# Optimization experiments

Measured on AMD Instinct MI355X. Metric: run time of the kernel, lower is better.

The kernel has to match this reference:

```python
import jax, jax.numpy as jnp
import numpy as np

K = 2          # top-k experts per token
CVLOSS = 0.0
SWITCHLOSS = 0.01
ZLOSS = 0.001
EPS = 1e-6


def setup_inputs() -> dict:
    key = jax.random.key(0)
    ks = jax.random.split(key, 4)
    B, L, D, H, E = 4, 2048, 512, 1024, 8
    x = jax.random.normal(ks[0], (B, L, D), dtype=jnp.float32)
    w_gate = jax.random.normal(ks[1], (E, D), dtype=jnp.float32) * 0.02
    w1 = jax.random.normal(ks[2], (E, D, H), dtype=jnp.float32) * (1.0 / np.sqrt(D))
    b1 = jnp.zeros((E, H), dtype=jnp.float32)
    w2 = jax.random.normal(ks[3], (E, H, D), dtype=jnp.float32) * (1.0 / np.sqrt(H))
    b2 = jnp.zeros((E, D), dtype=jnp.float32)
    return {"x": x, "w_gate": w_gate, "w1": w1, "b1": b1, "w2": w2, "b2": b2}


def _moe_forward(x, w_gate, w1, b1, w2, b2):
    B, L, D = x.shape
    E = w_gate.shape[0]
    xf = x.reshape(-1, D)                      # [N, D]
    N = xf.shape[0]

    # --- top-k gating (eval path: sample_topk=0, no skip_mask, concat=False) ---
    logits = xf @ w_gate.T                     # [N, E]
    probs = jax.nn.softmax(logits, axis=1)
    top_k_gates, top_k_idx = jax.lax.top_k(probs, K)        # [N, K]
    denom = jax.lax.stop_gradient(top_k_gates.sum(axis=1, keepdims=True) + EPS)
    top_k_gates = top_k_gates / denom
    gates = jnp.zeros_like(probs).at[jnp.arange(N)[:, None], top_k_idx].set(top_k_gates)  # [N, E]

    # --- auxiliary losses ---
    psum = probs.sum(axis=0)
    psum_n = psum / psum.sum()                 # F.normalize(p=1)
    freqs = (gates > 0).astype(probs.dtype).sum(axis=0)
    freqs_n = freqs / freqs.sum()
    cv = jnp.var(psum_n, ddof=1) / (jnp.mean(psum_n) ** 2 + 1e-10)
    switch = (psum_n * freqs_n).sum() * E
    zl = jnp.mean(jax.nn.logsumexp(logits, axis=1) ** 2)
    loss = CVLOSS * cv + SWITCHLOSS * switch + ZLOSS * zl

    # --- dispatch / per-expert FFN / gate-weighted combine ---
    # Mathematically identical to SparseDispatcher: tokens with gates[n,e]==0
    # contribute exactly zero for expert e. Loop is over the small fixed set
    # of experts, keeping intermediates at [N, H] (as the original does per group).
    y = jnp.zeros_like(xf)
    for e in range(E):
        h = jax.nn.relu(xf @ w1[e] + b1[e])    # [N, H]
        y = y + gates[:, e:e + 1] * (h @ w2[e] + b2[e])
    return y.reshape(B, L, D), loss


def reference(x, w_gate, w1, b1, w2, b2):
    return _moe_forward(x, w_gate, w1, b1, w2, b2)
```

## Files before the change

kernel.cpp:

```cpp
#include <hip/hip_runtime.h>
#include <hip/hip_bf16.h>
#include <math.h>

#define NTOK 8192
#define DDIM 512
#define HDIM 1024
#define NEXP 8
#define TOPK 2
#define NBLK_GATE (NTOK / 4)

typedef __bf16 bf16;
typedef __attribute__((ext_vector_type(8))) __bf16 bf16x8;
typedef __attribute__((ext_vector_type(4))) float f32x4;

#define WS_PSUM_PART_OFF  4096
#define WS_ZL_PART_OFF    (WS_PSUM_PART_OFF + NBLK_GATE * NEXP * 4)
#define WS_GATES_OFF      (WS_ZL_PART_OFF + NBLK_GATE * 4)
#define WS_LIST_OFF       (WS_GATES_OFF + NTOK * TOPK * 4)
#define WS_XB_OFF         (WS_LIST_OFF + NEXP * NTOK * 4)
#define WS_W1T_OFF        (WS_XB_OFF + NTOK * DDIM * 2)
#define WS_W2T_OFF        (WS_W1T_OFF + NEXP * DDIM * HDIM * 2)
#define WS_HB_OFF         (WS_W2T_OFF + NEXP * DDIM * HDIM * 2)

#define GL2LDS(g, l) __builtin_amdgcn_global_load_lds( \
    (const __attribute__((address_space(1))) void*)(g), \
    (__attribute__((address_space(3))) void*)(l), 16, 0, 0)

__global__ __launch_bounds__(256)
void gate_kernel(const float* __restrict__ x, const float* __restrict__ wg,
                 int* __restrict__ counts, float* __restrict__ psum_part,
                 float* __restrict__ zl_part, float* __restrict__ gates,
                 int* __restrict__ list, bf16* __restrict__ xb) {
    __shared__ float wls[NEXP * DDIM];
    __shared__ float blk_psum[NEXP];
    __shared__ float blk_zl;
    const int t = threadIdx.x;

    for (int i = t; i < NEXP * DDIM / 4; i += 256)
        ((float4*)wls)[i] = ((const float4*)wg)[i];
    if (t < NEXP) blk_psum[t] = 0.f;
    if (t == 0) blk_zl = 0.f;
    __syncthreads();

    const int wave = t >> 6, lane = t & 63;
    const int n = blockIdx.x * 4 + wave;

    const float* xr = x + (size_t)n * DDIM;

    {
        const float4 v0 = ((const float4*)xr)[lane * 2];
        const float4 v1 = ((const float4*)xr)[lane * 2 + 1];
        bf16x8 bv;
        bv[0] = (bf16)v0.x; bv[1] = (bf16)v0.y; bv[2] = (bf16)v0.z; bv[3] = (bf16)v0.w;
        bv[4] = (bf16)v1.x; bv[5] = (bf16)v1.y; bv[6] = (bf16)v1.z; bv[7] = (bf16)v1.w;
        *(bf16x8*)(xb + (size_t)n * DDIM + lane * 8) = bv;
    }

    float acc[NEXP];
#pragma unroll
    for (int e = 0; e < NEXP; ++e) acc[e] = 0.f;
#pragma unroll
    for (int it = 0; it < DDIM / 64; ++it) {
        const float xv = xr[lane + 64 * it];
#pragma unroll
        for (int e = 0; e < NEXP; ++e)
            acc[e] = fmaf(xv, wls[e * DDIM + lane + 64 * it], acc[e]);
    }
#pragma unroll
    for (int e = 0; e < NEXP; ++e) {
#pragma unroll
        for (int off = 32; off > 0; off >>= 1)
            acc[e] += __shfl_xor(acc[e], off);
    }

    float m = acc[0];
#pragma unroll
    for (int e = 1; e < NEXP; ++e) m = fmaxf(m, acc[e]);
    float p[NEXP];
    float se = 0.f;
#pragma unroll
    for (int e = 0; e < NEXP; ++e) { p[e] = expf(acc[e] - m); se += p[e]; }
    const float lse = m + logf(se);
    const float inv = 1.f / se;
#pragma unroll
    for (int e = 0; e < NEXP; ++e) p[e] *= inv;

    int e0 = 0; float g0 = p[0];
#pragma unroll
    for (int e = 1; e < NEXP; ++e) if (p[e] > g0) { g0 = p[e]; e0 = e; }
    int e1 = -1; float g1 = -1.f;
#pragma unroll
    for (int e = 0; e < NEXP; ++e) if (e != e0 && p[e] > g1) { g1 = p[e]; e1 = e; }
    const float denom = g0 + g1 + 1e-6f;

    if (lane == 0) {
        gates[n * 2 + 0] = g0 / denom;
        gates[n * 2 + 1] = g1 / denom;
        const int p0 = atomicAdd(&counts[e0 * 64], 1);
        list[e0 * NTOK + p0] = n * 2 + 0;
        const int p1 = atomicAdd(&counts[e1 * 64], 1);
        list[e1 * NTOK + p1] = n * 2 + 1;
#pragma unroll
        for (int e = 0; e < NEXP; ++e) atomicAdd(&blk_psum[e], p[e]);
        atomicAdd(&blk_zl, lse * lse);
    }
    __syncthreads();
    if (t < NEXP) psum_part[blockIdx.x * NEXP + t] = blk_psum[t];
    if (t == 0) zl_part[blockIdx.x] = blk_zl;
}

template <int R, int C>
__global__ __launch_bounds__(256)
void transpose_cvt(const float* __restrict__ in, bf16* __restrict__ outp) {
    __shared__ float tile[32][33];
    const int e = blockIdx.z;
    const int x0 = blockIdx.x * 32;
    const int y0 = blockIdx.y * 32;
    const int tx = threadIdx.x & 31, ty = threadIdx.x >> 5;
    const float* ip = in + (size_t)e * R * C;
    bf16* op = outp + (size_t)e * R * C;
#pragma unroll
    for (int q = 0; q < 4; ++q)
        tile[ty + q * 8][tx] = ip[(size_t)(y0 + ty + q * 8) * C + x0 + tx];
    __syncthreads();
#pragma unroll
    for (int q = 0; q < 4; ++q)
        op[(size_t)(x0 + ty + q * 8) * R + y0 + tx] = (bf16)tile[tx][ty + q * 8];
}

template <int KD, int ND, bool PASS2>
__global__ __launch_bounds__(256)
void ffn_mfma(const bf16* __restrict__ A_src, const bf16* __restrict__ Wt,
              const float* __restrict__ bias, const int* __restrict__ counts,
              const int* __restrict__ list, const float* __restrict__ gates,
              float* __restrict__ y_out, bf16* __restrict__ h_out) {
    const int e = blockIdx.z;
    const int cnt = counts[e * 64];
    const int row0 = blockIdx.y * 128;
    if (row0 >= cnt) return;
    const int col0 = blockIdx.x * 128;

    __shared__ __align__(16) short As[2][128 * 64];
    __shared__ __align__(16) short Bs[2][128 * 64];
    __shared__ int   ls_entry[128];
    __shared__ float ls_gate[128];

    const int t = threadIdx.x;
    const int lane = t & 63;
    const int w = t >> 6;

    if (t < 128) {
        const int r = row0 + t;
        const int entry = (r < cnt) ? list[e * NTOK + r] : -1;
        ls_entry[t] = entry;
        ls_gate[t] = (PASS2 && entry >= 0) ? gates[entry] : 0.f;
    }
    __syncthreads();

    const int subrow = lane >> 3;
    const int swzoff = ((lane & 7) ^ subrow) * 16;
    const char* Ab = (const char*)A_src;
    const char* Bb = (const char*)Wt;
    size_t a_row_byte[4], b_row_byte[4];
#pragma unroll
    for (int q = 0; q < 4; ++q) {
        const int r = q * 32 + w * 8 + subrow;
        const int entry = ls_entry[r];
        const int src = entry < 0 ? 0 : (PASS2 ? entry : (entry >> 1));
        a_row_byte[q] = (size_t)src * KD * 2;
        b_row_byte[q] = ((size_t)e * ND + col0 + r) * KD * 2;
    }
    const int lds_wbase = w * 8 * 128;

    f32x4 acc[4][4];
#pragma unroll
    for (int i = 0; i < 4; ++i)
#pragma unroll
        for (int j = 0; j < 4; ++j) acc[i][j] = (f32x4){0.f, 0.f, 0.f, 0.f};

    const int rowblk = (w >> 1) * 64;
    const int colblk = (w & 1) * 64;
    const int fr = lane & 15;
    const int kg = lane >> 4;

    auto STAGE = [&](int buf, int k0) {
        const size_t koff = (size_t)k0 * 2 + swzoff;
        char* ab = (char*)As + buf * 16384 + lds_wbase;
        char* bb = (char*)Bs + buf * 16384 + lds_wbase;
#pragma unroll
        for (int q = 0; q < 4; ++q) {
            GL2LDS(Ab + a_row_byte[q] + koff, ab + q * 32 * 128);
            GL2LDS(Bb + b_row_byte[q] + koff, bb + q * 32 * 128);
        }
    };

    auto COMPUTE = [&](int buf) {
        const char* AsB = (const char*)As + buf * 16384;
        const char* BsB = (const char*)Bs + buf * 16384;
#pragma unroll
        for (int kk = 0; kk < 2; ++kk) {
            bf16x8 af[4], bg[4];
#pragma unroll
            for (int i = 0; i < 4; ++i) {
                const int ra = rowblk + i * 16 + fr;
                const int ca = (kk * 4 + kg) ^ (ra & 7);
                af[i] = *(const bf16x8*)(AsB + ra * 128 + ca * 16);
                const int rb = colblk + i * 16 + fr;
                const int cb = (kk * 4 + kg) ^ (rb & 7);
                bg[i] = *(const bf16x8*)(BsB + rb * 128 + cb * 16);
            }
#pragma unroll
            for (int i = 0; i < 4; ++i)
#pragma unroll
                for (int j = 0; j < 4; ++j)
                    acc[i][j] = __builtin_amdgcn_mfma_f32_16x16x32_bf16(
                        af[i], bg[j], acc[i][j], 0, 0, 0);
        }
    };

    constexpr int NT = KD / 64;
    STAGE(0, 0);
    __syncthreads();
    for (int kt = 0; kt < NT - 1; ++kt) {
        STAGE((kt + 1) & 1, (kt + 1) * 64);
        COMPUTE(kt & 1);
        __syncthreads();
    }
    COMPUTE((NT - 1) & 1);

    float bcol[4];
#pragma unroll
    for (int j = 0; j < 4; ++j)
        bcol[j] = bias[e * ND + col0 + colblk + j * 16 + fr];

#pragma unroll
    for (int i = 0; i < 4; ++i) {
#pragma unroll
        for (int rg = 0; rg < 4; ++rg) {
            const int r = rowblk + i * 16 + kg * 4 + rg;
            const int entry = ls_entry[r];
            if (entry < 0) continue;
            if (!PASS2) {
                bf16* hr = h_out + (size_t)entry * HDIM + col0 + colblk + fr;
#pragma unroll
                for (int j = 0; j < 4; ++j)
                    hr[j * 16] = (bf16)fmaxf(acc[i][j][rg] + bcol[j], 0.f);
            } else {
                const float g = ls_gate[r];
                float* yr = y_out + (size_t)(entry >> 1) * DDIM + col0 + colblk + fr;
#pragma unroll
                for (int j = 0; j < 4; ++j)
                    atomicAdd(&yr[j * 16], g * (acc[i][j][rg] + bcol[j]));
            }
        }
    }
}

__global__ __launch_bounds__(256)
void finalize_kernel(const int* __restrict__ counts,
                     const float* __restrict__ psum_part,
                     const float* __restrict__ zl_part,
                     float* __restrict__ outp) {
    __shared__ float sp[NEXP];
    __shared__ float sz;
    const int t = threadIdx.x;
    if (t < NEXP) sp[t] = 0.f;
    if (t == 0) sz = 0.f;
    __syncthreads();
    float pe[NEXP] = {0.f, 0.f, 0.f, 0.f, 0.f, 0.f, 0.f, 0.f};
    float z = 0.f;
    for (int b = t; b < NBLK_GATE; b += 256) {
#pragma unroll
        for (int e = 0; e < NEXP; ++e) pe[e] += psum_part[b * NEXP + e];
        z += zl_part[b];
    }
#pragma unroll
    for (int e = 0; e < NEXP; ++e) atomicAdd(&sp[e], pe[e]);
    atomicAdd(&sz, z);
    __syncthreads();
    if (t == 0) {
        float S = 0.f;
        for (int e = 0; e < NEXP; ++e) S += sp[e];
        const float F = (float)(NTOK * TOPK);
        float sw = 0.f;
        for (int e = 0; e < NEXP; ++e)
            sw += (sp[e] / S) * ((float)counts[e * 64] / F);
        sw *= (float)NEXP;
        const float zl = sz / (float)NTOK;
        outp[(size_t)NTOK * DDIM] = 0.01f * sw + 0.001f * zl;
    }
}

extern "C" void kernel_launch(void* const* d_in, const int* in_sizes, int n_in,
                              void* d_out, int out_size, void* d_ws, size_t ws_size,
                              hipStream_t stream) {
    (void)in_sizes; (void)n_in; (void)out_size; (void)ws_size;
    const float* x  = (const float*)d_in[0];
    const float* wg = (const float*)d_in[1];
    const float* w1 = (const float*)d_in[2];
    const float* b1 = (const float*)d_in[3];
    const float* w2 = (const float*)d_in[4];
    const float* b2 = (const float*)d_in[5];
    float* y = (float*)d_out;

    char* ws = (char*)d_ws;
    int*   counts    = (int*)(ws + 0);
    float* psum_part = (float*)(ws + WS_PSUM_PART_OFF);
    float* zl_part   = (float*)(ws + WS_ZL_PART_OFF);
    float* gates     = (float*)(ws + WS_GATES_OFF);
    int*   list      = (int*)(ws + WS_LIST_OFF);
    bf16*  xb        = (bf16*)(ws + WS_XB_OFF);
    bf16*  w1t       = (bf16*)(ws + WS_W1T_OFF);
    bf16*  w2t       = (bf16*)(ws + WS_W2T_OFF);
    bf16*  hb        = (bf16*)(ws + WS_HB_OFF);

    hipMemsetAsync(ws, 0, 4096, stream);
    hipMemsetAsync(d_out, 0, (size_t)NTOK * DDIM * sizeof(float), stream);

    transpose_cvt<DDIM, HDIM><<<dim3(HDIM / 32, DDIM / 32, NEXP), 256, 0, stream>>>(w1, w1t);
    transpose_cvt<HDIM, DDIM><<<dim3(DDIM / 32, HDIM / 32, NEXP), 256, 0, stream>>>(w2, w2t);

    gate_kernel<<<NBLK_GATE, 256, 0, stream>>>(x, wg, counts, psum_part, zl_part,
                                               gates, list, xb);

    ffn_mfma<DDIM, HDIM, false>
        <<<dim3(HDIM / 128, NTOK / 128, NEXP), 256, 0, stream>>>(
            xb, w1t, b1, counts, list, gates, nullptr, hb);

    ffn_mfma<HDIM, DDIM, true>
        <<<dim3(DDIM / 128, NTOK / 128, NEXP), 256, 0, stream>>>(
            hb, w2t, b2, counts, list, gates, y, nullptr);

    finalize_kernel<<<1, 256, 0, stream>>>(counts, psum_part, zl_part, y);
}
```

Baseline: 260.4 us.

## Pack routed tokens contiguously per expert and compact the FFN grid

Adds a plan kernel that builds per-expert cumulative offsets and a compact list of (expert, row-block) tiles, and a pack kernel that gathers routed token rows into a contiguous bf16 buffer in expert-sorted slot order. Both FFN GEMMs then launch only the needed row blocks (RBMAX) rather than a full NTOK/128 x NEXP grid of mostly empty blocks, and read contiguous A rows without per-row indirection. The list is stored as 16-bit indices. This adds two small launches, including a single-thread serial plan kernel, and per-row list and gate loads in the PASS2 epilogue.

```diff
diff --git a/kernel.cpp b/kernel.cpp
--- a/kernel.cpp
+++ b/kernel.cpp
@@ -7,20 +7,25 @@
 #define HDIM 1024
 #define NEXP 8
 #define TOPK 2
+#define TOTSLOT (NTOK * TOPK)
 #define NBLK_GATE (NTOK / 4)
+#define RBMAX 144
 
 typedef __bf16 bf16;
 typedef __attribute__((ext_vector_type(8))) __bf16 bf16x8;
 typedef __attribute__((ext_vector_type(4))) float f32x4;
 
+#define WS_CUMOFF_OFF     2048
+#define WS_RBE_OFF        2112
+#define WS_RBR_OFF        2688
 #define WS_PSUM_PART_OFF  4096
-#define WS_ZL_PART_OFF    (WS_PSUM_PART_OFF + NBLK_GATE * NEXP * 4)
-#define WS_GATES_OFF      (WS_ZL_PART_OFF + NBLK_GATE * 4)
-#define WS_LIST_OFF       (WS_GATES_OFF + NTOK * TOPK * 4)
-#define WS_XB_OFF         (WS_LIST_OFF + NEXP * NTOK * 4)
-#define WS_W1T_OFF        (WS_XB_OFF + NTOK * DDIM * 2)
-#define WS_W2T_OFF        (WS_W1T_OFF + NEXP * DDIM * HDIM * 2)
-#define WS_HB_OFF         (WS_W2T_OFF + NEXP * DDIM * HDIM * 2)
+#define WS_ZL_PART_OFF    69632
+#define WS_GATES_OFF      77824
+#define WS_LIST_OFF       143360
+#define WS_XG_OFF         274432
+#define WS_W1T_OFF        17051648
+#define WS_W2T_OFF        25440256
+#define WS_HB_OFF         33828864
 
 #define GL2LDS(g, l) __builtin_amdgcn_global_load_lds( \
     (const __attribute__((address_space(1))) void*)(g), \
@@ -30,7 +35,7 @@
 void gate_kernel(const float* __restrict__ x, const float* __restrict__ wg,
                  int* __restrict__ counts, float* __restrict__ psum_part,
                  float* __restrict__ zl_part, float* __restrict__ gates,
-                 int* __restrict__ list, bf16* __restrict__ xb) {
+                 unsigned short* __restrict__ list) {
     __shared__ float wls[NEXP * DDIM];
     __shared__ float blk_psum[NEXP];
     __shared__ float blk_zl;
@@ -44,17 +49,7 @@
 
     const int wave = t >> 6, lane = t & 63;
     const int n = blockIdx.x * 4 + wave;
-
     const float* xr = x + (size_t)n * DDIM;
-
-    {
-        const float4 v0 = ((const float4*)xr)[lane * 2];
-        const float4 v1 = ((const float4*)xr)[lane * 2 + 1];
-        bf16x8 bv;
-        bv[0] = (bf16)v0.x; bv[1] = (bf16)v0.y; bv[2] = (bf16)v0.z; bv[3] = (bf16)v0.w;
-        bv[4] = (bf16)v1.x; bv[5] = (bf16)v1.y; bv[6] = (bf16)v1.z; bv[7] = (bf16)v1.w;
-        *(bf16x8*)(xb + (size_t)n * DDIM + lane * 8) = bv;
-    }
 
     float acc[NEXP];
 #pragma unroll
@@ -97,9 +92,9 @@
         gates[n * 2 + 0] = g0 / denom;
         gates[n * 2 + 1] = g1 / denom;
         const int p0 = atomicAdd(&counts[e0 * 64], 1);
-        list[e0 * NTOK + p0] = n * 2 + 0;
+        list[e0 * NTOK + p0] = (unsigned short)(n * 2 + 0);
         const int p1 = atomicAdd(&counts[e1 * 64], 1);
-        list[e1 * NTOK + p1] = n * 2 + 1;
+        list[e1 * NTOK + p1] = (unsigned short)(n * 2 + 1);
 #pragma unroll
         for (int e = 0; e < NEXP; ++e) atomicAdd(&blk_psum[e], p[e]);
         atomicAdd(&blk_zl, lse * lse);
@@ -107,6 +102,40 @@
     __syncthreads();
     if (t < NEXP) psum_part[blockIdx.x * NEXP + t] = blk_psum[t];
     if (t == 0) zl_part[blockIdx.x] = blk_zl;
+}
+
+__global__ void plan_kernel(const int* __restrict__ counts, int* __restrict__ cumoff,
+                            int* __restrict__ rb_e, int* __restrict__ rb_r) {
+    if (threadIdx.x == 0 && blockIdx.x == 0) {
+        int off = 0, idx = 0;
+        for (int e = 0; e < NEXP; ++e) {
+            cumoff[e] = off;
+            const int c = counts[e * 64];
+            off += c;
+            for (int r = 0; r < c; r += 128) { rb_e[idx] = e; rb_r[idx] = r; ++idx; }
+        }
+        cumoff[NEXP] = off;
+        for (; idx < RBMAX; ++idx) { rb_e[idx] = -1; rb_r[idx] = 0; }
+    }
+}
+
+__global__ __launch_bounds__(256)
+void pack_kernel(const float* __restrict__ x, const unsigned short* __restrict__ list,
+                 const int* __restrict__ cumoff, bf16* __restrict__ xg) {
+    const int wave = threadIdx.x >> 6, lane = threadIdx.x & 63;
+    const int slot = blockIdx.x * 4 + wave;
+    int e = 0;
+#pragma unroll
+    for (int k = 1; k < NEXP; ++k) e += (slot >= cumoff[k]) ? 1 : 0;
+    const int pos = slot - cumoff[e];
+    const int entry = list[e * NTOK + pos];
+    const int n = entry >> 1;
+    const float4 v0 = ((const float4*)(x + (size_t)n * DDIM))[lane * 2];
+    const float4 v1 = ((const float4*)(x + (size_t)n * DDIM))[lane * 2 + 1];
+    bf16x8 bv;
+    bv[0] = (bf16)v0.x; bv[1] = (bf16)v0.y; bv[2] = (bf16)v0.z; bv[3] = (bf16)v0.w;
+    bv[4] = (bf16)v1.x; bv[5] = (bf16)v1.y; bv[6] = (bf16)v1.z; bv[7] = (bf16)v1.w;
+    *(bf16x8*)(xg + (size_t)slot * DDIM + lane * 8) = bv;
 }
 
 template <int R, int C>
@@ -132,30 +161,23 @@
 __global__ __launch_bounds__(256)
 void ffn_mfma(const bf16* __restrict__ A_src, const bf16* __restrict__ Wt,
               const float* __restrict__ bias, const int* __restrict__ counts,
-              const int* __restrict__ list, const float* __restrict__ gates,
+              const int* __restrict__ cumoff, const int* __restrict__ rb_e,
+              const int* __restrict__ rb_r, const unsigned short* __restrict__ list,
+              const float* __restrict__ gates,
               float* __restrict__ y_out, bf16* __restrict__ h_out) {
-    const int e = blockIdx.z;
+    const int e = rb_e[blockIdx.y];
+    if (e < 0) return;
+    const int row0 = rb_r[blockIdx.y];
     const int cnt = counts[e * 64];
-    const int row0 = blockIdx.y * 128;
-    if (row0 >= cnt) return;
+    const int slotbase = cumoff[e] + row0;
     const int col0 = blockIdx.x * 128;
 
     __shared__ __align__(16) short As[2][128 * 64];
     __shared__ __align__(16) short Bs[2][128 * 64];
-    __shared__ int   ls_entry[128];
-    __shared__ float ls_gate[128];
 
     const int t = threadIdx.x;
     const int lane = t & 63;
     const int w = t >> 6;
-
-    if (t < 128) {
-        const int r = row0 + t;
-        const int entry = (r < cnt) ? list[e * NTOK + r] : -1;
-        ls_entry[t] = entry;
-        ls_gate[t] = (PASS2 && entry >= 0) ? gates[entry] : 0.f;
-    }
-    __syncthreads();
 
     const int subrow = lane >> 3;
     const int swzoff = ((lane & 7) ^ subrow) * 16;
@@ -165,9 +187,9 @@
 #pragma unroll
     for (int q = 0; q < 4; ++q) {
         const int r = q * 32 + w * 8 + subrow;
-        const int entry = ls_entry[r];
-        const int src = entry < 0 ? 0 : (PASS2 ? entry : (entry >> 1));
-        a_row_byte[q] = (size_t)src * KD * 2;
+        const int slot = slotbase + r;
+        const int sclamp = slot < TOTSLOT ? slot : TOTSLOT - 1;
+        a_row_byte[q] = (size_t)sclamp * KD * 2;
         b_row_byte[q] = ((size_t)e * ND + col0 + r) * KD * 2;
     }
     const int lds_wbase = w * 8 * 128;
@@ -238,15 +260,15 @@
 #pragma unroll
         for (int rg = 0; rg < 4; ++rg) {
             const int r = rowblk + i * 16 + kg * 4 + rg;
-            const int entry = ls_entry[r];
-            if (entry < 0) continue;
+            if (row0 + r >= cnt) continue;
             if (!PASS2) {
-                bf16* hr = h_out + (size_t)entry * HDIM + col0 + colblk + fr;
+                bf16* hr = h_out + (size_t)(slotbase + r) * HDIM + col0 + colblk + fr;
 #pragma unroll
                 for (int j = 0; j < 4; ++j)
                     hr[j * 16] = (bf16)fmaxf(acc[i][j][rg] + bcol[j], 0.f);
             } else {
-                const float g = ls_gate[r];
+                const int entry = list[e * NTOK + row0 + r];
+                const float g = gates[entry];
                 float* yr = y_out + (size_t)(entry >> 1) * DDIM + col0 + colblk + fr;
 #pragma unroll
                 for (int j = 0; j < 4; ++j)
@@ -305,11 +327,14 @@
 
     char* ws = (char*)d_ws;
     int*   counts    = (int*)(ws + 0);
+    int*   cumoff    = (int*)(ws + WS_CUMOFF_OFF);
+    int*   rb_e      = (int*)(ws + WS_RBE_OFF);
+    int*   rb_r      = (int*)(ws + WS_RBR_OFF);
     float* psum_part = (float*)(ws + WS_PSUM_PART_OFF);
     float* zl_part   = (float*)(ws + WS_ZL_PART_OFF);
     float* gates     = (float*)(ws + WS_GATES_OFF);
-    int*   list      = (int*)(ws + WS_LIST_OFF);
-    bf16*  xb        = (bf16*)(ws + WS_XB_OFF);
+    unsigned short* list = (unsigned short*)(ws + WS_LIST_OFF);
+    bf16*  xg        = (bf16*)(ws + WS_XG_OFF);
     bf16*  w1t       = (bf16*)(ws + WS_W1T_OFF);
     bf16*  w2t       = (bf16*)(ws + WS_W2T_OFF);
     bf16*  hb        = (bf16*)(ws + WS_HB_OFF);
@@ -321,15 +346,17 @@
     transpose_cvt<HDIM, DDIM><<<dim3(DDIM / 32, HDIM / 32, NEXP), 256, 0, stream>>>(w2, w2t);
 
     gate_kernel<<<NBLK_GATE, 256, 0, stream>>>(x, wg, counts, psum_part, zl_part,
-                                               gates, list, xb);
+                                               gates, list);
+    plan_kernel<<<1, 64, 0, stream>>>(counts, cumoff, rb_e, rb_r);
+    pack_kernel<<<TOTSLOT / 4, 256, 0, stream>>>(x, list, cumoff, xg);
 
     ffn_mfma<DDIM, HDIM, false>
-        <<<dim3(HDIM / 128, NTOK / 128, NEXP), 256, 0, stream>>>(
-            xb, w1t, b1, counts, list, gates, nullptr, hb);
+        <<<dim3(HDIM / 128, RBMAX), 256, 0, stream>>>(
+            xg, w1t, b1, counts, cumoff, rb_e, rb_r, list, gates, nullptr, hb);
 
     ffn_mfma<HDIM, DDIM, true>
-        <<<dim3(DDIM / 128, NTOK / 128, NEXP), 256, 0, stream>>>(
-            hb, w2t, b2, counts, list, gates, y, nullptr);
+        <<<dim3(DDIM / 128, RBMAX), 256, 0, stream>>>(
+            hb, w2t, b2, counts, cumoff, rb_e, rb_r, list, gates, y, nullptr);
 
     finalize_kernel<<<1, 256, 0, stream>>>(counts, psum_part, zl_part, y);
 }
```

Result: slower. 280.9 us (+7.9%).
